# Optimization experiments

Hardware: AMD Instinct MI355X
Metric: run time of the kernel (lower is better)

Reference implementation:

```python
import jax, jax.numpy as jnp
import numpy as np
import math

H, W, K = 512, 512, 16
B = 64


def _U(r2):
    # torch: r**2 * log(r**2 + 1e-6), with r = euclidean norm -> r2 = squared norm
    return r2 * jnp.log(r2 + 1e-6)


def _base_control_points():
    k_sqrt = int(math.sqrt(K))
    x = jnp.linspace(-1.0, 1.0, k_sqrt)
    y = jnp.linspace(-1.0, 1.0, k_sqrt)
    gx, gy = jnp.meshgrid(x, y, indexing='ij')  # torch default meshgrid is 'ij'
    return jnp.stack([gx.ravel(), gy.ravel()], axis=1)  # [K, 2]


def _target_grid():
    x = jnp.linspace(-1.0, 1.0, W)
    y = jnp.linspace(-1.0, 1.0, H)
    gy, gx = jnp.meshgrid(y, x, indexing='ij')
    return jnp.stack([gx.ravel(), gy.ravel()], axis=1)  # [H*W, 2]


def setup_inputs() -> dict:
    key = jax.random.key(0)
    source_points = jax.random.normal(key, (B, K, 2), dtype=jnp.float32)
    return {"source_points": source_points}


def reference(source_points):
    cp = _base_control_points()      # [K, 2]
    grid = _target_grid()            # [HW, 2]

    # Delta matrix (K+3, K+3). Diagonal of U-block is 0 (matches i != j loop since U(0)=0).
    d = cp[:, None, :] - cp[None, :, :]
    r2 = jnp.sum(d * d, axis=-1)
    Ukk = _U(r2)
    delta = jnp.zeros((K + 3, K + 3), dtype=source_points.dtype)
    delta = delta.at[:K, :K].set(Ukk)
    delta = delta.at[:K, K].set(1.0)
    delta = delta.at[:K, K + 1:].set(cp)
    delta = delta.at[K, :K].set(1.0)
    delta = delta.at[K + 1:, :K].set(cp.T)
    inv_delta = jnp.linalg.inv(delta)  # computed once, shared across batch

    # Batched coefficients: param matrix = [source_points ; zeros(3,2)]
    Pm = jnp.concatenate(
        [source_points, jnp.zeros((source_points.shape[0], 3, 2), dtype=source_points.dtype)],
        axis=1,
    )  # [B, K+3, 2]
    coeff = jnp.einsum('ij,bjd->bid', inv_delta, Pm)  # [B, K+3, 2]

    # RBF basis for target grid (batch-independent): [HW, K]
    dg = grid[:, None, :] - cp[None, :, :]
    Ug = _U(jnp.sum(dg * dg, axis=-1))
    # Affine part: [1, x, y]
    Pg = jnp.concatenate([jnp.ones((grid.shape[0], 1), dtype=grid.dtype), grid], axis=1)  # [HW, 3]

    out = jnp.einsum('nk,bkd->bnd', Ug, coeff[:, :K, :]) + jnp.einsum('nt,btd->bnd', Pg, coeff[:, K:, :])
    return out.reshape(source_points.shape[0], H, W, 2)
```

## Files before the change

### kernel.cpp

```cpp
#include <hip/hip_runtime.h>

#define HH 512
#define WW 512
#define BB 64
#define HW (HH*WW)
#define CSTRIDE 40
#define BGRP 16

typedef float v2f __attribute__((ext_vector_type(2)));
typedef float v4f __attribute__((ext_vector_type(4)));

constexpr double cx_ln(double x) {
  int e = 0;
  while (x >= 2.0) { x *= 0.5; ++e; }
  while (x < 1.0)  { x *= 2.0; --e; }
  double z = (x - 1.0) / (x + 1.0);
  double z2 = z * z, term = z, sum = 0.0;
  for (int n = 1; n < 60; n += 2) { sum += term / n; term *= z2; }
  return 2.0 * sum + e * 0.69314718055994530942;
}

struct WMat { float w[19][16]; };

constexpr WMat build_wm() {
  const double Xc[4] = {-1.0, -1.0/3.0, 1.0/3.0, 1.0};
  double A[19][38] = {};
  for (int r = 0; r < 19; ++r) {
    for (int c = 0; c < 38; ++c) {
      double v = 0.0;
      if (c >= 19) {
        v = ((c - 19) == r) ? 1.0 : 0.0;
      } else if (r < 16 && c < 16) {
        double dx = Xc[r >> 2] - Xc[c >> 2];
        double dy = Xc[r & 3] - Xc[c & 3];
        double r2 = dx * dx + dy * dy;
        v = (r2 == 0.0) ? 0.0 : r2 * cx_ln(r2 + 1e-6);
      } else if (r < 16) {
        v = (c == 16) ? 1.0 : ((c == 17) ? Xc[r >> 2] : Xc[r & 3]);
      } else if (c < 16) {
        v = (r == 16) ? 1.0 : ((r == 17) ? Xc[c >> 2] : Xc[c & 3]);
      }
      A[r][c] = v;
    }
  }
  for (int k = 0; k < 19; ++k) {
    int best = k;
    double bv = A[k][k] < 0 ? -A[k][k] : A[k][k];
    for (int r = k + 1; r < 19; ++r) {
      double av = A[r][k] < 0 ? -A[r][k] : A[r][k];
      if (av > bv) { bv = av; best = r; }
    }
    if (best != k)
      for (int c = 0; c < 38; ++c) { double t = A[k][c]; A[k][c] = A[best][c]; A[best][c] = t; }
    double rp = 1.0 / A[k][k];
    for (int c = 0; c < 38; ++c) A[k][c] *= rp;
    for (int r = 0; r < 19; ++r) {
      if (r == k) continue;
      double f = A[r][k];
      for (int c = 0; c < 38; ++c) A[r][c] -= f * A[k][c];
    }
  }
  WMat wm = {};
  for (int i = 0; i < 19; ++i)
    for (int j = 0; j < 16; ++j)
      wm.w[i][j] = (float)(A[i][19 + j] * (i < 16 ? 0.69314718055994530942 : 1.0));
  return wm;
}

__device__ __constant__ WMat WM = build_wm();

__device__ __forceinline__ float fast_log2(float x) {
#if __has_builtin(__builtin_amdgcn_logf)
  return __builtin_amdgcn_logf(x);
#else
  return __log2f(x);
#endif
}

__global__ __launch_bounds__(64) void tps_coeff_kernel(
    const float* __restrict__ sp, float* __restrict__ coeff) {
  const int b = blockIdx.x;
  const int tid = threadIdx.x;
  if (tid < 38) {
    const int i = tid >> 1, d = tid & 1;
    const float* s = sp + b * 32 + d;
    float acc = 0.0f;
#pragma unroll
    for (int j = 0; j < 16; ++j) acc = fmaf(WM.w[i][j], s[2 * j], acc);
    coeff[b * CSTRIDE + tid] = acc;
  }
}

__global__ __launch_bounds__(256) void tps_grid_kernel(
    const float* __restrict__ coeff, float* __restrict__ out) {
  const int n0 = (blockIdx.x * 256 + threadIdx.x) * 2;
  const int ix = n0 & (WW - 1);
  const int iy = n0 >> 9;
  const float step = 2.0f / 511.0f;
  const float gy = -1.0f + iy * step;
  const v2f gxv = {-1.0f + ix * step, -1.0f + (ix + 1) * step};
  const float Xc[4] = {-1.0f, -1.0f / 3.0f, 1.0f / 3.0f, 1.0f};

  float dy2[4];
#pragma unroll
  for (int j = 0; j < 4; ++j) { float t = gy - Xc[j]; dy2[j] = t * t; }

  v2f dxp[4];
#pragma unroll
  for (int i = 0; i < 4; ++i) {
    v2f t = gxv - Xc[i];
    dxp[i] = t * t + 1e-6f;
  }

  v2f u2[16];
#pragma unroll
  for (int k = 0; k < 16; ++k) {
    v2f t = dxp[k >> 2] + dy2[k & 3];
    u2[k] = t * (v2f){fast_log2(t.x), fast_log2(t.y)};
  }

  const int b0 = blockIdx.y * BGRP;
  for (int bi = 0; bi < BGRP; ++bi) {
    const int b = b0 + bi;
    const float* __restrict__ c = coeff + b * CSTRIDE;
    float cc[38];
#pragma unroll
    for (int i = 0; i < 38; ++i) cc[i] = c[i];

    v2f accx = cc[32] + gxv * cc[34] + gy * cc[36];
    v2f accy = cc[33] + gxv * cc[35] + gy * cc[37];
#pragma unroll
    for (int k = 0; k < 16; ++k) {
      accx += u2[k] * cc[2 * k];
      accy += u2[k] * cc[2 * k + 1];
    }

    v4f v = {accx.x, accy.x, accx.y, accy.y};
    __builtin_nontemporal_store(v, (v4f*)(out + (size_t)(b * HW + n0) * 2));
  }
}

extern "C" void kernel_launch(void* const* d_in, const int* in_sizes, int n_in,
                              void* d_out, int out_size, void* d_ws, size_t ws_size,
                              hipStream_t stream) {
  const float* sp = (const float*)d_in[0];
  float* out = (float*)d_out;
  float* coeff = (float*)d_ws;

  tps_coeff_kernel<<<BB, 64, 0, stream>>>(sp, coeff);

  dim3 grid(HW / 512, BB / BGRP);
  tps_grid_kernel<<<grid, 256, 0, stream>>>(coeff, out);
}
```

Measured before the change: 140.5 us.

## Fuse coefficient computation into grid kernel via shared memory

Removes the separate coefficient kernel: each block recomputes the coefficients for its 16 batches into shared memory, then reads them back as vector loads. This drops one launch and the global round trip for the coefficients. In exchange every block repeats the small 16x16 matvec and adds a barrier. The nontemporal output stores also become plain stores.

```diff
diff --git a/kernel.cpp b/kernel.cpp
--- a/kernel.cpp
+++ b/kernel.cpp
@@ -4,7 +4,6 @@
 #define WW 512
 #define BB 64
 #define HW (HH*WW)
-#define CSTRIDE 40
 #define BGRP 16
 
 typedef float v2f __attribute__((ext_vector_type(2)));
@@ -77,22 +76,22 @@
 #endif
 }
 
-__global__ __launch_bounds__(64) void tps_coeff_kernel(
-    const float* __restrict__ sp, float* __restrict__ coeff) {
-  const int b = blockIdx.x;
-  const int tid = threadIdx.x;
-  if (tid < 38) {
-    const int i = tid >> 1, d = tid & 1;
-    const float* s = sp + b * 32 + d;
+__global__ __launch_bounds__(256) void tps_fused_kernel(
+    const float* __restrict__ sp, float* __restrict__ out) {
+  __shared__ float lc[BGRP][40];
+  const int b0 = blockIdx.y * BGRP;
+
+  for (int e = threadIdx.x; e < BGRP * 38; e += 256) {
+    const int bi = e / 38;
+    const int idx = e - bi * 38;
+    const int row = idx >> 1, d = idx & 1;
+    const float* s = sp + (b0 + bi) * 32 + d;
     float acc = 0.0f;
 #pragma unroll
-    for (int j = 0; j < 16; ++j) acc = fmaf(WM.w[i][j], s[2 * j], acc);
-    coeff[b * CSTRIDE + tid] = acc;
+    for (int j = 0; j < 16; ++j) acc = fmaf(WM.w[row][j], s[2 * j], acc);
+    lc[bi][idx] = acc;
   }
-}
 
-__global__ __launch_bounds__(256) void tps_grid_kernel(
-    const float* __restrict__ coeff, float* __restrict__ out) {
   const int n0 = (blockIdx.x * 256 + threadIdx.x) * 2;
   const int ix = n0 & (WW - 1);
   const int iy = n0 >> 9;
@@ -119,24 +118,28 @@
     u2[k] = t * (v2f){fast_log2(t.x), fast_log2(t.y)};
   }
 
-  const int b0 = blockIdx.y * BGRP;
+  __syncthreads();
+
+  float* op = out + (size_t)(b0 * (size_t)HW + n0) * 2;
   for (int bi = 0; bi < BGRP; ++bi) {
-    const int b = b0 + bi;
-    const float* __restrict__ c = coeff + b * CSTRIDE;
-    float cc[38];
+    const v4f* c4 = (const v4f*)lc[bi];
+    v4f q[10];
 #pragma unroll
-    for (int i = 0; i < 38; ++i) cc[i] = c[i];
+    for (int i = 0; i < 10; ++i) q[i] = c4[i];
+#define CQ(i) (q[(i) >> 2][(i) & 3])
 
-    v2f accx = cc[32] + gxv * cc[34] + gy * cc[36];
-    v2f accy = cc[33] + gxv * cc[35] + gy * cc[37];
+    v2f accx = CQ(32) + gxv * CQ(34) + gy * CQ(36);
+    v2f accy = CQ(33) + gxv * CQ(35) + gy * CQ(37);
 #pragma unroll
     for (int k = 0; k < 16; ++k) {
-      accx += u2[k] * cc[2 * k];
-      accy += u2[k] * cc[2 * k + 1];
+      accx += u2[k] * CQ(2 * k);
+      accy += u2[k] * CQ(2 * k + 1);
     }
+#undef CQ
 
     v4f v = {accx.x, accy.x, accx.y, accy.y};
-    __builtin_nontemporal_store(v, (v4f*)(out + (size_t)(b * HW + n0) * 2));
+    *(v4f*)op = v;
+    op += (size_t)HW * 2;
   }
 }
 
@@ -145,10 +148,8 @@
                               hipStream_t stream) {
   const float* sp = (const float*)d_in[0];
   float* out = (float*)d_out;
-  float* coeff = (float*)d_ws;
-
-  tps_coeff_kernel<<<BB, 64, 0, stream>>>(sp, coeff);
+  (void)d_ws; (void)ws_size;
 
   dim3 grid(HW / 512, BB / BGRP);
-  tps_grid_kernel<<<grid, 256, 0, stream>>>(coeff, out);
+  tps_fused_kernel<<<grid, 256, 0, stream>>>(sp, out);
 }
```

After: 137.1 us. 2.4% less time.

## Process four rows per thread with swizzled block order and regular stores

Applied to the files above, without the earlier changes.

Each thread now computes the radial basis for four image rows instead of one. That cuts the grid from 512 blocks to 128 along x and amortises the per-batch coefficient loads across four rows. The block index is swizzled so that consecutive launched blocks cover different batch groups and row ranges. The nontemporal stores are replaced with ordinary vector stores. In exchange, register use rises (64 v2f basis values plus accumulators) and there are fewer blocks, which may hurt occupancy and latency hiding on a kernel bound by output writes.

```diff
diff --git a/kernel.cpp b/kernel.cpp
--- a/kernel.cpp
+++ b/kernel.cpp
@@ -93,17 +93,15 @@
 
 __global__ __launch_bounds__(256) void tps_grid_kernel(
     const float* __restrict__ coeff, float* __restrict__ out) {
-  const int n0 = (blockIdx.x * 256 + threadIdx.x) * 2;
-  const int ix = n0 & (WW - 1);
-  const int iy = n0 >> 9;
+  const int lin = blockIdx.y * 128 + blockIdx.x;
+  const int swz = (lin & 7) * 64 + (lin >> 3);
+  const int bx = swz & 127, by = swz >> 7;
+  const int tid = threadIdx.x;
+  const int ix = 2 * tid;
+  const int b0 = by * BGRP;
   const float step = 2.0f / 511.0f;
-  const float gy = -1.0f + iy * step;
   const v2f gxv = {-1.0f + ix * step, -1.0f + (ix + 1) * step};
   const float Xc[4] = {-1.0f, -1.0f / 3.0f, 1.0f / 3.0f, 1.0f};
-
-  float dy2[4];
-#pragma unroll
-  for (int j = 0; j < 4; ++j) { float t = gy - Xc[j]; dy2[j] = t * t; }
 
   v2f dxp[4];
 #pragma unroll
@@ -112,31 +110,54 @@
     dxp[i] = t * t + 1e-6f;
   }
 
-  v2f u2[16];
+  float gy4[4];
+  v2f u[4][16];
 #pragma unroll
-  for (int k = 0; k < 16; ++k) {
-    v2f t = dxp[k >> 2] + dy2[k & 3];
-    u2[k] = t * (v2f){fast_log2(t.x), fast_log2(t.y)};
+  for (int j = 0; j < 4; ++j) {
+    const float gy = -1.0f + (bx * 4 + j) * step;
+    gy4[j] = gy;
+    float dy2[4];
+#pragma unroll
+    for (int i = 0; i < 4; ++i) { float t = gy - Xc[i]; dy2[i] = t * t; }
+#pragma unroll
+    for (int k = 0; k < 16; ++k) {
+      v2f t = dxp[k >> 2] + dy2[k & 3];
+      u[j][k] = t * (v2f){fast_log2(t.x), fast_log2(t.y)};
+    }
   }
 
-  const int b0 = blockIdx.y * BGRP;
+  float* op[4];
+#pragma unroll
+  for (int j = 0; j < 4; ++j)
+    op[j] = out + ((size_t)b0 * HW + (size_t)(bx * 4 + j) * WW + ix) * 2;
+
   for (int bi = 0; bi < BGRP; ++bi) {
-    const int b = b0 + bi;
-    const float* __restrict__ c = coeff + b * CSTRIDE;
+    const float* __restrict__ c = coeff + (b0 + bi) * CSTRIDE;
     float cc[38];
 #pragma unroll
     for (int i = 0; i < 38; ++i) cc[i] = c[i];
 
-    v2f accx = cc[32] + gxv * cc[34] + gy * cc[36];
-    v2f accy = cc[33] + gxv * cc[35] + gy * cc[37];
+    v2f ax[4], ay[4];
+#pragma unroll
+    for (int j = 0; j < 4; ++j) {
+      ax[j] = cc[32] + gxv * cc[34] + gy4[j] * cc[36];
+      ay[j] = cc[33] + gxv * cc[35] + gy4[j] * cc[37];
+    }
 #pragma unroll
     for (int k = 0; k < 16; ++k) {
-      accx += u2[k] * cc[2 * k];
-      accy += u2[k] * cc[2 * k + 1];
+#pragma unroll
+      for (int j = 0; j < 4; ++j) {
+        ax[j] += u[j][k] * cc[2 * k];
+        ay[j] += u[j][k] * cc[2 * k + 1];
+      }
     }
 
-    v4f v = {accx.x, accy.x, accx.y, accy.y};
-    __builtin_nontemporal_store(v, (v4f*)(out + (size_t)(b * HW + n0) * 2));
+#pragma unroll
+    for (int j = 0; j < 4; ++j) {
+      v4f v = {ax[j].x, ay[j].x, ax[j].y, ay[j].y};
+      *(v4f*)op[j] = v;
+      op[j] += (size_t)HW * 2;
+    }
   }
 }
 
@@ -149,6 +170,6 @@
 
   tps_coeff_kernel<<<BB, 64, 0, stream>>>(sp, coeff);
 
-  dim3 grid(HW / 512, BB / BGRP);
+  dim3 grid(128, BB / BGRP);
   tps_grid_kernel<<<grid, 256, 0, stream>>>(coeff, out);
 }
```

Measured after the change: 136.4 us. 2.9% less time.
